# Optimization experiments

Hardware: AMD Instinct MI355X
Metric: run time of the kernel (lower is better)

The kernel has to match this reference:

```python
import jax, jax.numpy as jnp
import numpy as np

IOU_THRESHOLD = 0.5  # default iou_threshold of nms/class_spec_nms


def _nms_keep_mask(boxes, scores, iou_threshold):
    """Faithful port of the hand-rolled greedy NMS.

    The torch version builds a variable-length index list; here we return the
    equivalent fixed-shape boolean keep mask over the N boxes (jit-friendly).
    """
    n = scores.shape[0]
    x1, y1, x2, y2 = boxes[:, 0], boxes[:, 1], boxes[:, 2], boxes[:, 3]
    areas = (x2 - x1) * (y2 - y1)                       # [N]
    # pairwise intersection via broadcasted min/max (same math as the matmul-
    # with-ones trick in the source, without materializing the ones matrices)
    xi = jnp.minimum(x2[:, None], x2[None, :]) - jnp.maximum(x1[:, None], x1[None, :])
    yi = jnp.minimum(y2[:, None], y2[None, :]) - jnp.maximum(y1[:, None], y1[None, :])
    inter = jnp.maximum(xi, 0.0) * jnp.maximum(yi, 0.0)  # [N,N]
    iou = inter / (areas[:, None] + areas[None, :] - inter)

    first_max = scores.max()
    first_min = scores.min()
    curr_idx0 = jnp.argmax(scores)

    # carry: (candidate mask, working scores copy, keep mask, curr max, curr idx)
    init = (scores < first_max, scores, jnp.zeros((n,), dtype=bool), first_max, curr_idx0)

    def cond(state):
        mask, _, _, cmax, _ = state
        return jnp.any(mask) & (cmax >= first_min)

    def body(state):
        mask, sc, keep, cmax, cidx = state
        mask = mask & (iou[cidx] <= iou_threshold)   # suppress overlaps with current max
        mask = mask.at[cidx].set(False)
        keep = keep.at[cidx].set(True)               # keep current max
        sc = jnp.where(mask, sc, first_min - 1.0)    # kill suppressed scores
        cidx = jnp.argmax(sc)
        return mask, sc, keep, sc[cidx], cidx

    _, _, keep, _, _ = jax.lax.while_loop(cond, body, init)
    return keep


def setup_inputs() -> dict:
    key = jax.random.key(0)
    k1, k2, k3, k4, k5, k6 = jax.random.split(key, 6)
    N = 4096    # pre-NMS candidate boxes
    L = 16384   # p3 locations for a 1024x1024 image at stride 8 (128*128)
    xy = jax.random.uniform(k1, (N, 2), dtype=jnp.float32) * 900.0
    wh = jax.random.uniform(k2, (N, 2), dtype=jnp.float32) * 100.0 + 1.0
    boxes = jnp.concatenate([xy, xy + wh], axis=1)          # valid x1<x2, y1<y2
    scores = jax.random.uniform(k3, (N,), dtype=jnp.float32)
    class_ids = jax.random.randint(k4, (N,), 0, 80, dtype=jnp.int32)
    locations = jax.random.uniform(k5, (L, 2), dtype=jnp.float32) * 1024.0
    deltas = jax.random.uniform(k6, (L, 4), dtype=jnp.float32)  # positive gt deltas
    return {"boxes": boxes, "scores": scores, "class_ids": class_ids,
            "locations": locations, "deltas": deltas, "stride": 8}


def reference(boxes, scores, class_ids, locations, deltas, stride):
    # ---- class_spec_nms: class-offset trick then plain NMS ----
    max_coordinate = boxes.max()
    offsets = class_ids.astype(boxes.dtype) * (max_coordinate + 1.0)
    boxes_for_nms = boxes + offsets[:, None]
    keep_mask = _nms_keep_mask(boxes_for_nms, scores, IOU_THRESHOLD)

    # ---- fcos_apply_deltas_to_locations ----
    clipped = jnp.maximum(deltas, 0.0)
    s = jnp.asarray(stride, dtype=deltas.dtype)
    px, py = locations[:, 0], locations[:, 1]
    pred_boxes = jnp.stack([px - clipped[:, 0] * s,
                            py - clipped[:, 1] * s,
                            px + clipped[:, 2] * s,
                            py + clipped[:, 3] * s], axis=1)  # [L,4]

    # ---- fcos_make_centerness_targets ----
    lr_min = jnp.minimum(deltas[:, 0], deltas[:, 2])
    tb_min = jnp.minimum(deltas[:, 1], deltas[:, 3])
    lr_max = jnp.maximum(deltas[:, 0], deltas[:, 2])
    tb_max = jnp.maximum(deltas[:, 1], deltas[:, 3])
    centerness = jnp.sqrt((lr_min * tb_min) / (lr_max * tb_max))
    centerness = jnp.where(jnp.all(deltas == -1.0, axis=1), -1.0, centerness)

    pred_out = jnp.concatenate([pred_boxes, centerness[:, None]], axis=1)  # [L,5]
    return keep_mask, pred_out
```

## Files before the change

### kernel.cpp

```cpp
#include <hip/hip_runtime.h>
#include <stdint.h>

#define NB 4096
#define NBLK 64
#define LLOC 16384
#define IOU_THR 0.5f
#define ECAP 1024
#define RANKB 256
#define NTRI (NBLK * (NBLK + 1) / 2)

typedef unsigned long long u64;

__device__ __forceinline__ u64 readlane64(u64 v, int lane) {
    unsigned lo = (unsigned)__builtin_amdgcn_readlane((int)(unsigned)(v & 0xffffffffull), lane);
    unsigned hi = (unsigned)__builtin_amdgcn_readlane((int)(unsigned)(v >> 32), lane);
    return ((u64)hi << 32) | (u64)lo;
}

__global__ void __launch_bounds__(256) fused_front(
        const float* __restrict__ boxes, const float* __restrict__ scores,
        const float* __restrict__ loc, const float* __restrict__ deltas,
        const int* __restrict__ stride_p,
        float* __restrict__ pred_out, float* __restrict__ maxc,
        int* __restrict__ sidx, int* __restrict__ counts) {
    __shared__ __align__(16) float sh[NB];
    __shared__ float red[4];
    int blk = blockIdx.x;
    int t = threadIdx.x;

    if (blk < 64) {
        int i = blk * 256 + t;
        float s = (float)stride_p[0];
        float2 p = ((const float2*)loc)[i];
        float4 d = ((const float4*)deltas)[i];
        float c0 = fmaxf(d.x, 0.f), c1 = fmaxf(d.y, 0.f);
        float c2 = fmaxf(d.z, 0.f), c3 = fmaxf(d.w, 0.f);
        float b0 = p.x - c0 * s;
        float b1 = p.y - c1 * s;
        float b2 = p.x + c2 * s;
        float b3 = p.y + c3 * s;
        float lr_min = fminf(d.x, d.z), tb_min = fminf(d.y, d.w);
        float lr_max = fmaxf(d.x, d.z), tb_max = fmaxf(d.y, d.w);
        float cent = sqrtf((lr_min * tb_min) / (lr_max * tb_max));
        if (d.x == -1.f && d.y == -1.f && d.z == -1.f && d.w == -1.f) cent = -1.f;
        float* o = pred_out + (size_t)i * 5;
        o[0] = b0; o[1] = b1; o[2] = b2; o[3] = b3; o[4] = cent;
    } else if (blk < 64 + RANKB) {
        for (int i = t; i < NB; i += 256) sh[i] = scores[i];
        __syncthreads();
        int wave = t >> 6, lane = t & 63;
        int base = (blk - 64) * 16 + wave * 4;
        float my0 = sh[base + 0], my1 = sh[base + 1];
        float my2 = sh[base + 2], my3 = sh[base + 3];
        int c0 = 0, c1 = 0, c2 = 0, c3 = 0;
#pragma unroll 8
        for (int k = 0; k < 64; ++k) {
            int j = lane + k * 64;
            float sj = sh[j];
            c0 += (sj > my0) || (sj == my0 && j < base + 0);
            c1 += (sj > my1) || (sj == my1 && j < base + 1);
            c2 += (sj > my2) || (sj == my2 && j < base + 2);
            c3 += (sj > my3) || (sj == my3 && j < base + 3);
        }
        for (int o = 32; o > 0; o >>= 1) {
            c0 += __shfl_down(c0, o); c1 += __shfl_down(c1, o);
            c2 += __shfl_down(c2, o); c3 += __shfl_down(c3, o);
        }
        if (lane == 0) {
            sidx[c0] = base + 0; sidx[c1] = base + 1;
            sidx[c2] = base + 2; sidx[c3] = base + 3;
        }
    } else {
        if (t < NBLK) counts[t] = 0;
        float m = -3.0e38f;
        for (int i = t; i < NB * 4; i += 256) m = fmaxf(m, boxes[i]);
        for (int o = 32; o > 0; o >>= 1) m = fmaxf(m, __shfl_down(m, o));
        if ((t & 63) == 0) red[t >> 6] = m;
        __syncthreads();
        if (t == 0) *maxc = fmaxf(fmaxf(red[0], red[1]), fmaxf(red[2], red[3]));
    }
}

__global__ void __launch_bounds__(64) edge_kernel(
        const float* __restrict__ boxes, const int* __restrict__ cls,
        const float* __restrict__ maxc, const int* __restrict__ sidx,
        int* __restrict__ counts, uint4* __restrict__ entries) {
    int idx = blockIdx.x, r = 0;
    while (idx >= NBLK - r) { idx -= NBLK - r; ++r; }
    int c = r + idx;

    __shared__ float4 cb[64];
    __shared__ float ca[64];
    int t = threadIdx.x;
    float mc1 = maxc[0] + 1.0f;

    int jr = sidx[r * 64 + t];
    float offr = (float)cls[jr] * mc1;
    float4 rb = ((const float4*)boxes)[jr];
    rb.x += offr; rb.y += offr; rb.z += offr; rb.w += offr;
    float ra = (rb.z - rb.x) * (rb.w - rb.y);

    if (c == r) {
        cb[t] = rb; ca[t] = ra;
    } else {
        int jc = sidx[c * 64 + t];
        float offc = (float)cls[jc] * mc1;
        float4 b = ((const float4*)boxes)[jc];
        b.x += offc; b.y += offc; b.z += offc; b.w += offc;
        cb[t] = b; ca[t] = (b.z - b.x) * (b.w - b.y);
    }
    __syncthreads();

    u64 w = 0;
#pragma unroll 8
    for (int j = 0; j < 64; ++j) {
        float4 b = cb[j];
        float xi = fminf(rb.z, b.z) - fmaxf(rb.x, b.x);
        float yi = fminf(rb.w, b.w) - fmaxf(rb.y, b.y);
        float inter = fmaxf(xi, 0.f) * fmaxf(yi, 0.f);
        float iou = inter / (ra + ca[j] - inter);
        w |= (u64)(iou > IOU_THR) << j;
    }
    if (c == r) w &= ~(1ull << t);
    if (w) {
        int slot = atomicAdd(&counts[r], 1);
        if (slot < ECAP)
            entries[r * ECAP + slot] =
                make_uint4((unsigned)(t | (c << 8)), 0u,
                           (unsigned)(w & 0xffffffffull), (unsigned)(w >> 32));
    }
}

__global__ void __launch_bounds__(64) scan_kernel(
        const int* __restrict__ counts, const uint4* __restrict__ entries,
        const int* __restrict__ sidx, float* __restrict__ keep_out) {
    const int lane = threadIdx.x;
    int cnt_l = counts[lane];
    u64 accv = 0;
    u64 keptall = 0;
    u64 self = 1ull << lane;

    uint4 cur = entries[lane];
    uint4 n1  = entries[ECAP + lane];
    for (int b = 0; b < NBLK; ++b) {
        uint4 n2;
        if (b < NBLK - 2) n2 = entries[(u64)(b + 2) * ECAP + lane];

        int cnt = __builtin_amdgcn_readlane(cnt_l, b);
        if (cnt > ECAP) cnt = ECAP;
        int cfast = cnt < 64 ? cnt : 64;

        u64 colw = self;
        for (int e = 0; e < cfast; ++e) {
            unsigned meta = (unsigned)__builtin_amdgcn_readlane((int)cur.x, e);
            int l = meta & 255, c = meta >> 8;
            if (c == b) {
                unsigned lo = (unsigned)__builtin_amdgcn_readlane((int)cur.z, e);
                unsigned hi = (unsigned)__builtin_amdgcn_readlane((int)cur.w, e);
                if (lane == l) colw |= ((u64)hi << 32) | lo;
            }
        }
        for (int e = 64; e < cnt; ++e) {
            uint4 x = entries[(u64)b * ECAP + e];
            int l = x.x & 255, c = x.x >> 8;
            if (c == b && lane == l) colw |= ((u64)x.w << 32) | x.z;
        }

        u64 rem = readlane64(accv, b);
        u64 avail = ~rem;
        u64 edges = colw & avail & ~self;
        u64 involved = __ballot(edges != 0ull) & avail;
        u64 keptm = avail & ~involved;
        u64 sub = involved;
        while (sub) {
            int i = (int)__builtin_ctzll(sub);
            keptm |= 1ull << i;
            u64 ci = readlane64(colw, i);
            sub &= ~(ci | (1ull << i));
        }
        if (lane == b) keptall = keptm;

        for (int e = 0; e < cfast; ++e) {
            unsigned meta = (unsigned)__builtin_amdgcn_readlane((int)cur.x, e);
            unsigned lo   = (unsigned)__builtin_amdgcn_readlane((int)cur.z, e);
            unsigned hi   = (unsigned)__builtin_amdgcn_readlane((int)cur.w, e);
            int l = meta & 255, c = meta >> 8;
            if (((keptm >> l) & 1ull) && lane == c) accv |= ((u64)hi << 32) | lo;
        }
        for (int e = 64; e < cnt; ++e) {
            uint4 x = entries[(u64)b * ECAP + e];
            int l = x.x & 255, c = x.x >> 8;
            if (((keptm >> l) & 1ull) && lane == c) accv |= ((u64)x.w << 32) | x.z;
        }
        cur = n1; n1 = n2;
    }

#pragma unroll 8
    for (int bb = 0; bb < NBLK; ++bb) {
        u64 kw = readlane64(keptall, bb);
        int idx = sidx[bb * 64 + lane];
        keep_out[idx] = ((kw >> lane) & 1ull) ? 1.0f : 0.0f;
    }
}

extern "C" void kernel_launch(void* const* d_in, const int* in_sizes, int n_in,
                              void* d_out, int out_size, void* d_ws, size_t ws_size,
                              hipStream_t stream) {
    const float* boxes   = (const float*)d_in[0];
    const float* scores  = (const float*)d_in[1];
    const int*   cls     = (const int*)d_in[2];
    const float* loc     = (const float*)d_in[3];
    const float* deltas  = (const float*)d_in[4];
    const int*   stride  = (const int*)d_in[5];

    float* out = (float*)d_out;
    float* keep_out = out;
    float* pred_out = out + NB;

    char* ws = (char*)d_ws;
    float* maxc    = (float*)ws;                     ws += 16;
    int*   sidx    = (int*)ws;                       ws += NB * sizeof(int);
    int*   counts  = (int*)ws;                       ws += NBLK * sizeof(int) + 16;
    uint4* entries = (uint4*)ws;

    fused_front<<<64 + RANKB + 1, 256, 0, stream>>>(boxes, scores, loc, deltas, stride,
                                                    pred_out, maxc, sidx, counts);
    edge_kernel<<<NTRI, 64, 0, stream>>>(boxes, cls, maxc, sidx, counts, entries);
    scan_kernel<<<1, 64, 0, stream>>>(counts, entries, sidx, keep_out);
}
```

Before: 109.9 us.

## Store diagonal NMS blocks densely and apply suppression via LDS atomicOr

The edge kernel now writes diagonal-block overlap masks into a dense per-block array instead of the atomic entry list, so the serial scan no longer has to filter entries to rebuild its in-block column words. The scan spreads the suppression masks of kept boxes in parallel with LDS atomicOr on a per-block removal array, replacing the per-entry readlane loops, and it prefetches the dense masks two blocks ahead. The final keep write is spread across four waves. The cost is LDS atomics and an extra workspace array, in exchange for a shorter serial critical path.

```diff
diff --git a/kernel.cpp b/kernel.cpp
--- a/kernel.cpp
+++ b/kernel.cpp
@@ -84,7 +84,8 @@
 __global__ void __launch_bounds__(64) edge_kernel(
         const float* __restrict__ boxes, const int* __restrict__ cls,
         const float* __restrict__ maxc, const int* __restrict__ sidx,
-        int* __restrict__ counts, uint4* __restrict__ entries) {
+        int* __restrict__ counts, uint4* __restrict__ entries,
+        u64* __restrict__ dcol) {
     int idx = blockIdx.x, r = 0;
     while (idx >= NBLK - r) { idx -= NBLK - r; ++r; }
     int c = r + idx;
@@ -121,8 +122,10 @@
         float iou = inter / (ra + ca[j] - inter);
         w |= (u64)(iou > IOU_THR) << j;
     }
-    if (c == r) w &= ~(1ull << t);
-    if (w) {
+    if (c == r) {
+        w &= ~(1ull << t);
+        dcol[r * 64 + t] = w;
+    } else if (w) {
         int slot = atomicAdd(&counts[r], 1);
         if (slot < ECAP)
             entries[r * ECAP + slot] =
@@ -131,73 +134,76 @@
     }
 }
 
-__global__ void __launch_bounds__(64) scan_kernel(
+__global__ void __launch_bounds__(256) scan_kernel(
         const int* __restrict__ counts, const uint4* __restrict__ entries,
-        const int* __restrict__ sidx, float* __restrict__ keep_out) {
-    const int lane = threadIdx.x;
-    int cnt_l = counts[lane];
-    u64 accv = 0;
-    u64 keptall = 0;
-    u64 self = 1ull << lane;
-
-    uint4 cur = entries[lane];
-    uint4 n1  = entries[ECAP + lane];
-    for (int b = 0; b < NBLK; ++b) {
-        uint4 n2;
-        if (b < NBLK - 2) n2 = entries[(u64)(b + 2) * ECAP + lane];
-
-        int cnt = __builtin_amdgcn_readlane(cnt_l, b);
-        if (cnt > ECAP) cnt = ECAP;
-        int cfast = cnt < 64 ? cnt : 64;
-
-        u64 colw = self;
-        for (int e = 0; e < cfast; ++e) {
-            unsigned meta = (unsigned)__builtin_amdgcn_readlane((int)cur.x, e);
-            int l = meta & 255, c = meta >> 8;
-            if (c == b) {
-                unsigned lo = (unsigned)__builtin_amdgcn_readlane((int)cur.z, e);
-                unsigned hi = (unsigned)__builtin_amdgcn_readlane((int)cur.w, e);
-                if (lane == l) colw |= ((u64)hi << 32) | lo;
-            }
-        }
-        for (int e = 64; e < cnt; ++e) {
-            uint4 x = entries[(u64)b * ECAP + e];
-            int l = x.x & 255, c = x.x >> 8;
-            if (c == b && lane == l) colw |= ((u64)x.w << 32) | x.z;
-        }
-
-        u64 rem = readlane64(accv, b);
-        u64 avail = ~rem;
-        u64 edges = colw & avail & ~self;
-        u64 involved = __ballot(edges != 0ull) & avail;
-        u64 keptm = avail & ~involved;
-        u64 sub = involved;
-        while (sub) {
-            int i = (int)__builtin_ctzll(sub);
-            keptm |= 1ull << i;
-            u64 ci = readlane64(colw, i);
-            sub &= ~(ci | (1ull << i));
-        }
-        if (lane == b) keptall = keptm;
-
-        for (int e = 0; e < cfast; ++e) {
-            unsigned meta = (unsigned)__builtin_amdgcn_readlane((int)cur.x, e);
-            unsigned lo   = (unsigned)__builtin_amdgcn_readlane((int)cur.z, e);
-            unsigned hi   = (unsigned)__builtin_amdgcn_readlane((int)cur.w, e);
-            int l = meta & 255, c = meta >> 8;
-            if (((keptm >> l) & 1ull) && lane == c) accv |= ((u64)hi << 32) | lo;
-        }
-        for (int e = 64; e < cnt; ++e) {
-            uint4 x = entries[(u64)b * ECAP + e];
-            int l = x.x & 255, c = x.x >> 8;
-            if (((keptm >> l) & 1ull) && lane == c) accv |= ((u64)x.w << 32) | x.z;
-        }
-        cur = n1; n1 = n2;
-    }
-
-#pragma unroll 8
-    for (int bb = 0; bb < NBLK; ++bb) {
-        u64 kw = readlane64(keptall, bb);
+        const u64* __restrict__ dcol, const int* __restrict__ sidx,
+        float* __restrict__ keep_out) {
+    __shared__ u64 rem_lds[NBLK];
+    __shared__ u64 kept_lds[NBLK];
+    const int t = threadIdx.x;
+    const int lane = t & 63;
+
+    if (t < 64) {
+        rem_lds[t] = 0;
+        int cnt_l = counts[lane];
+        u64 keptall_w = 0;
+        u64 self = 1ull << lane;
+
+        uint4 cur = entries[lane];
+        uint4 n1  = entries[ECAP + lane];
+        u64 cw_cur = dcol[lane];
+        u64 cw_n1  = dcol[64 + lane];
+        for (int b = 0; b < NBLK; ++b) {
+            uint4 n2; u64 cw_n2;
+            if (b < NBLK - 2) {
+                n2    = entries[(u64)(b + 2) * ECAP + lane];
+                cw_n2 = dcol[(b + 2) * 64 + lane];
+            }
+
+            int cnt = __builtin_amdgcn_readlane(cnt_l, b);
+            if (cnt > ECAP) cnt = ECAP;
+
+            u64 colw = self | cw_cur;
+
+            u64 rem = rem_lds[b];
+            u64 avail = ~rem;
+            u64 edges = colw & avail & ~self;
+            u64 involved = __ballot(edges != 0ull) & avail;
+            u64 keptm = avail & ~involved;
+            u64 sub = involved;
+            while (sub) {
+                int i = (int)__builtin_ctzll(sub);
+                keptm |= 1ull << i;
+                u64 ci = readlane64(colw, i);
+                sub &= ~(ci | (1ull << i));
+            }
+            if (lane == b) keptall_w = keptm;
+
+            if (lane < cnt) {
+                int l = cur.x & 255, c = cur.x >> 8;
+                if ((keptm >> l) & 1ull)
+                    atomicOr(&rem_lds[c], ((u64)cur.w << 32) | cur.z);
+            }
+            for (int e = 64; e < cnt; e += 64) {
+                int ee = e + lane;
+                if (ee < cnt) {
+                    uint4 x = entries[(u64)b * ECAP + ee];
+                    int l = x.x & 255, c = x.x >> 8;
+                    if ((keptm >> l) & 1ull)
+                        atomicOr(&rem_lds[c], ((u64)x.w << 32) | x.z);
+                }
+            }
+            cur = n1; n1 = n2; cw_cur = cw_n1; cw_n1 = cw_n2;
+        }
+        kept_lds[lane] = keptall_w;
+    }
+    __syncthreads();
+
+    int w = t >> 6;
+#pragma unroll
+    for (int k = 0; k < 16; ++k) {
+        int bb = w + k * 4;
+        u64 kw = kept_lds[bb];
         int idx = sidx[bb * 64 + lane];
         keep_out[idx] = ((kw >> lane) & 1ull) ? 1.0f : 0.0f;
     }
@@ -221,10 +227,11 @@
     float* maxc    = (float*)ws;                     ws += 16;
     int*   sidx    = (int*)ws;                       ws += NB * sizeof(int);
     int*   counts  = (int*)ws;                       ws += NBLK * sizeof(int) + 16;
-    uint4* entries = (uint4*)ws;
+    uint4* entries = (uint4*)ws;                     ws += (size_t)NBLK * ECAP * sizeof(uint4);
+    u64*   dcol    = (u64*)ws;
 
     fused_front<<<64 + RANKB + 1, 256, 0, stream>>>(boxes, scores, loc, deltas, stride,
                                                     pred_out, maxc, sidx, counts);
-    edge_kernel<<<NTRI, 64, 0, stream>>>(boxes, cls, maxc, sidx, counts, entries);
-    scan_kernel<<<1, 64, 0, stream>>>(counts, entries, sidx, keep_out);
-}
+    edge_kernel<<<NTRI, 64, 0, stream>>>(boxes, cls, maxc, sidx, counts, entries, dcol);
+    scan_kernel<<<1, 256, 0, stream>>>(counts, entries, dcol, sidx, keep_out);
+}
```

Result: no change. 108.4 us (-1.4%).
